# Performance work log

Hardware: AMD Instinct MI355X
Metric: run time of the kernel (lower is better)

The kernel has to match this reference:

```python
import jax, jax.numpy as jnp
from jax import lax
import numpy as np

SEQ, FEAT, VOCAB = 59, 64, 578
B, U = 4096, 1024


def setup_inputs() -> dict:
    key = jax.random.key(0)
    ks = jax.random.split(key, 6)
    x = jax.random.normal(ks[0], (B, SEQ, FEAT), dtype=jnp.float32)
    # Keras LSTMCell params: kernel [feat, 4U], recurrent_kernel [U, 4U], bias [4U]
    kernel = jax.random.normal(ks[1], (FEAT, 4 * U), dtype=jnp.float32) * 0.05
    rec_kernel = jax.random.normal(ks[2], (U, 4 * U), dtype=jnp.float32) * 0.05
    bias = jnp.zeros((4 * U,), dtype=jnp.float32)
    w2 = jax.random.normal(ks[3], (U, VOCAB), dtype=jnp.float32) * 0.05
    b2 = jnp.zeros((VOCAB,), dtype=jnp.float32)
    return {"x": x, "kernel": kernel, "rec_kernel": rec_kernel, "bias": bias, "w2": w2, "b2": b2}


def reference(x, kernel, rec_kernel, bias, w2, b2):
    batch = x.shape[0]
    units = rec_kernel.shape[0]
    xs = jnp.transpose(x, (1, 0, 2))  # [SEQ, B, FEAT]
    h0 = jnp.zeros((batch, units), dtype=x.dtype)
    c0 = jnp.zeros((batch, units), dtype=x.dtype)

    def step(carry, xt):
        h, c = carry
        z = xt @ kernel + h @ rec_kernel + bias  # [B, 4U]
        i, f, g, o = jnp.split(z, 4, axis=-1)    # Keras gate order i,f,c,o
        i = jax.nn.sigmoid(i)
        f = jax.nn.sigmoid(f)
        g = jnp.tanh(g)
        o = jax.nn.sigmoid(o)
        c_new = f * c + i * g
        h_new = o * jnp.tanh(c_new)
        return (h_new, c_new), None

    (h_last, _), _ = lax.scan(step, (h0, c0), xs)
    probs = jax.nn.softmax(h_last @ w2 + b2, axis=-1)  # dense2 softmax on last hidden
    # original: stack single prediction -> [1,B,V], transpose [1,0,2] -> [B,1,V]
    return probs[:, None, :]
```

## Files before the change

kernel.cpp:

```cpp
#include <hip/hip_runtime.h>

#define SEQ    59
#define FEAT   64
#define VOCAB  578
#define BATCH  4096
#define UNITS  1024
#define KLSTM  1088
#define KPAD   1152
#define HSTRIDE 1088
#define NPAD   640

typedef __bf16 bf16x8 __attribute__((ext_vector_type(8)));
typedef __bf16 bf16x4 __attribute__((ext_vector_type(4)));
typedef float  floatx4 __attribute__((ext_vector_type(4)));

typedef const __attribute__((address_space(1))) char gas_char;
typedef __attribute__((address_space(3))) char las_char;

__device__ __forceinline__ float sigmoid_f(float x) { return 1.f / (1.f + __expf(-x)); }
__device__ __forceinline__ float tanh_f(float x) { float e = __expf(2.f * x); return 1.f - 2.f / (e + 1.f); }

#define GLDS(srcp, dstp) __builtin_amdgcn_global_load_lds((gas_char*)(srcp), (las_char*)(dstp), 16, 0, 0)
#define BAR()  __builtin_amdgcn_s_barrier()
#define LGKM0() asm volatile("s_waitcnt lgkmcnt(0)" ::: "memory")
#define VM6()  asm volatile("s_waitcnt vmcnt(6)" ::: "memory")
#define MFMA   __builtin_amdgcn_mfma_f32_16x16x32_bf16


__global__ void convert_x_kernel(const float* __restrict__ x, __bf16* __restrict__ xbf) {
    int i = blockIdx.x * 256 + threadIdx.x;
    const int total = BATCH * SEQ * FEAT / 4;
    if (i >= total) return;
    float4 v = ((const float4*)x)[i];
    bf16x4 o;
    o.x = (__bf16)v.x; o.y = (__bf16)v.y; o.z = (__bf16)v.z; o.w = (__bf16)v.w;
    ((bf16x4*)xbf)[i] = o;
}

__global__ void convert_weights_kernel(const float* __restrict__ kern,
                                       const float* __restrict__ reck,
                                       __bf16* __restrict__ Wtp) {
    int idx = blockIdx.x * 256 + threadIdx.x;
    if (idx >= 4096 * KPAD) return;
    int np = idx / KPAD;
    int k  = idx - np * KPAD;
    int bc = np >> 8;
    int w  = (np >> 6) & 3;
    int g  = (np >> 4) & 3;
    int j  = np & 15;
    int n  = g * 1024 + bc * 64 + w * 16 + j;
    float v = 0.f;
    if (k < FEAT)       v = kern[(size_t)k * 4096 + n];
    else if (k < KLSTM) v = reck[(size_t)(k - FEAT) * 4096 + n];
    Wtp[idx] = (__bf16)v;
}

__global__ void convert_w2_kernel(const float* __restrict__ w2, __bf16* __restrict__ Wt2p) {
    int idx = blockIdx.x * 256 + threadIdx.x;
    if (idx >= NPAD * 1024) return;
    int n = idx >> 10;
    int k = idx & 1023;
    float v = (n < VOCAB) ? w2[(size_t)k * VOCAB + n] : 0.f;
    Wt2p[idx] = (__bf16)v;
}

__global__ void __launch_bounds__(512, 2) lstm_step_kernel(
    const __bf16* __restrict__ xbf,
    const __bf16* __restrict__ Wtp,
    const float*  __restrict__ bias,
    const __bf16* __restrict__ hin,
    __bf16*       __restrict__ hout,
    float*        __restrict__ cstate,
    int t)
{
    __shared__ __bf16 Ash[2][2][256 * 32];
    __shared__ __bf16 Bsh[2][2][128 * 64];

    const int tid  = threadIdx.x;
    const int wid  = tid >> 6;
    const int lane = tid & 63;
    const int ln   = lane & 15;
    const int lk   = lane >> 4;
    const int wm   = wid >> 2;
    const int wn   = wid & 3;
    const int rb   = blockIdx.x;
    const int bc   = blockIdx.y;

    floatx4 acc[8][4];
#pragma unroll
    for (int m = 0; m < 8; ++m)
#pragma unroll
        for (int g = 0; g < 4; ++g)
            acc[m][g] = (floatx4){0.f, 0.f, 0.f, 0.f};

    const int af0 = tid, af1 = 512 + tid;
    const int ar0 = af0 >> 2, ar1 = af1 >> 2;
    const int ac0 = (af0 & 3) ^ ((ar0 >> 1) & 3);
    const int ac1 = (af1 & 3) ^ ((ar1 >> 1) & 3);
    const int br0 = af0 >> 3, br1 = af1 >> 3;
    const int bc0 = (af0 & 7) ^ (br0 & 7);
    const int bc1 = (af1 & 7) ^ (br1 & 7);

    const __bf16* hA0 = hin + (size_t)(rb * 256 + ar0) * HSTRIDE + ac0 * 8;
    const __bf16* hA1 = hin + (size_t)(rb * 256 + ar1) * HSTRIDE + ac1 * 8;
    const __bf16* xA0 = xbf + (size_t)(rb * 256 + ar0) * (SEQ * FEAT) + t * FEAT + ac0 * 8;
    const __bf16* xA1 = xbf + (size_t)(rb * 256 + ar1) * (SEQ * FEAT) + t * FEAT + ac1 * 8;
    const __bf16* wB0 = Wtp + (size_t)(bc * 256 + br0) * KPAD + bc0 * 8;
    const __bf16* wB1 = Wtp + (size_t)(bc * 256 + br1) * KPAD + bc1 * 8;

    const int adst0 = (wid << 9);
    const int adst1 = 4096 + (wid << 9);

#define STA(BUF, KH, COLB) do { \
    GLDS(hA0 + (COLB) + (KH) * 32, &Ash[BUF][KH][adst0]); \
    GLDS(hA1 + (COLB) + (KH) * 32, &Ash[BUF][KH][adst1]); } while (0)
#define STB(BUF, NH, COLB) do { \
    GLDS(wB0 + (size_t)(NH) * 128 * KPAD + (COLB), &Bsh[BUF][NH][adst0]); \
    GLDS(wB1 + (size_t)(NH) * 128 * KPAD + (COLB), &Bsh[BUF][NH][adst1]); } while (0)

    int offA[8];
#pragma unroll
    for (int m = 0; m < 8; ++m) {
        int row = wm * 128 + m * 16 + ln;
        offA[m] = row * 32 + ((lk ^ ((row >> 1) & 3)) << 3);
    }
    int offB[4][2];
#pragma unroll
    for (int g = 0; g < 4; ++g) {
        int nr = (wn & 1) * 64 + g * 16 + ln;
#pragma unroll
        for (int kk = 0; kk < 2; ++kk)
            offB[g][kk] = nr * 64 + ((((kk << 2) + lk) ^ (nr & 7)) << 3);
    }
    const int nhsel = wn >> 1;
    const __bf16* B0  = Bsh[0][nhsel];
    const __bf16* B1  = Bsh[1][nhsel];
    const __bf16* A00 = Ash[0][0];
    const __bf16* A01 = Ash[0][1];
    const __bf16* A10 = Ash[1][0];
    const __bf16* A11 = Ash[1][1];

    STB(0, 1, 0);
    GLDS(xA0, &Ash[0][0][adst0]); GLDS(xA1, &Ash[0][0][adst1]);
    STB(0, 0, 0);
    GLDS(xA0 + 32, &Ash[0][1][adst0]); GLDS(xA1 + 32, &Ash[0][1][adst1]);
    STB(1, 1, 64);
    STA(1, 0, 0);
    STB(1, 0, 64);
    VM6();
    BAR();

#define PHASE_MFMA(MB, KKB) \
    __builtin_amdgcn_s_setprio(1); \
    _Pragma("unroll") \
    for (int m = 0; m < 4; ++m) \
    _Pragma("unroll") \
        for (int g = 0; g < 4; ++g) \
            acc[(MB) + m][g] = MFMA(aa[m], bb[KKB][g], acc[(MB) + m][g], 0, 0, 0); \
    __builtin_amdgcn_s_setprio(0)

#pragma unroll 1
    for (int it = 0; it < 9; ++it) {
        const int t2 = (2 * it + 2 <= 17) ? (2 * it + 2) : 17;
        const int t3 = (2 * it + 3 <= 17) ? (2 * it + 3) : 17;
        const int cA1 = it * 128;
        const int cB2 = t2 * 64, cA2 = (t2 - 1) * 64;
        const int cB3 = t3 * 64, cA3 = (t3 - 1) * 64;
        bf16x8 bb[2][4], aa[4];

#pragma unroll
        for (int g = 0; g < 4; ++g) {
            bb[0][g] = *(const bf16x8*)(B0 + offB[g][0]);
            bb[1][g] = *(const bf16x8*)(B0 + offB[g][1]);
        }
#pragma unroll
        for (int m = 0; m < 4; ++m) aa[m] = *(const bf16x8*)(A00 + offA[m]);
        STA(1, 1, cA1);
        BAR(); LGKM0();
        PHASE_MFMA(0, 0);
        BAR();
#pragma unroll
        for (int m = 0; m < 4; ++m) aa[m] = *(const bf16x8*)(A00 + offA[4 + m]);
        STB(0, 1, cB2);
        BAR(); LGKM0();
        PHASE_MFMA(4, 0);
        BAR();
#pragma unroll
        for (int m = 0; m < 4; ++m) aa[m] = *(const bf16x8*)(A01 + offA[m]);
        STA(0, 0, cA2);
        BAR(); LGKM0();
        PHASE_MFMA(0, 1);
        BAR();
#pragma unroll
        for (int m = 0; m < 4; ++m) aa[m] = *(const bf16x8*)(A01 + offA[4 + m]);
        STB(0, 0, cB2);
        BAR(); LGKM0();
        PHASE_MFMA(4, 1);
        VM6();
        BAR();

#pragma unroll
        for (int g = 0; g < 4; ++g) {
            bb[0][g] = *(const bf16x8*)(B1 + offB[g][0]);
            bb[1][g] = *(const bf16x8*)(B1 + offB[g][1]);
        }
#pragma unroll
        for (int m = 0; m < 4; ++m) aa[m] = *(const bf16x8*)(A10 + offA[m]);
        STA(0, 1, cA2);
        BAR(); LGKM0();
        PHASE_MFMA(0, 0);
        BAR();
#pragma unroll
        for (int m = 0; m < 4; ++m) aa[m] = *(const bf16x8*)(A10 + offA[4 + m]);
        STB(1, 1, cB3);
        BAR(); LGKM0();
        PHASE_MFMA(4, 0);
        BAR();
#pragma unroll
        for (int m = 0; m < 4; ++m) aa[m] = *(const bf16x8*)(A11 + offA[m]);
        STA(1, 0, cA3);
        BAR(); LGKM0();
        PHASE_MFMA(0, 1);
        BAR();
#pragma unroll
        for (int m = 0; m < 4; ++m) aa[m] = *(const bf16x8*)(A11 + offA[4 + m]);
        STB(1, 0, cB3);
        BAR(); LGKM0();
        PHASE_MFMA(4, 1);
        VM6();
        BAR();
    }

    asm volatile("s_waitcnt vmcnt(0)" ::: "memory");

    const int u = bc * 64 + wn * 16 + ln;
    const float bi  = bias[u];
    const float bfv = bias[UNITS + u];
    const float bg  = bias[2 * UNITS + u];
    const float bo  = bias[3 * UNITS + u];
#pragma unroll
    for (int m = 0; m < 8; ++m) {
        const int row0 = rb * 256 + wm * 128 + m * 16 + lk * 4;
#pragma unroll
        for (int r = 0; r < 4; ++r) {
            const size_t ic = (size_t)(row0 + r) * UNITS + u;
            float ig = sigmoid_f(acc[m][0][r] + bi);
            float fg = sigmoid_f(acc[m][1][r] + bfv);
            float gg = tanh_f(acc[m][2][r] + bg);
            float og = sigmoid_f(acc[m][3][r] + bo);
            float cn = fg * cstate[ic] + ig * gg;
            cstate[ic] = cn;
            hout[(size_t)(row0 + r) * HSTRIDE + u] = (__bf16)(og * tanh_f(cn));
        }
    }
#undef STA
#undef STB
}

__global__ void __launch_bounds__(256) dense_kernel(
    const __bf16* __restrict__ hin,
    const __bf16* __restrict__ Wt2p,
    float*        __restrict__ logits)
{
    __shared__ __bf16 As[128 * 64];
    __shared__ __bf16 Bs[128 * 64];

    const int tid  = threadIdx.x;
    const int wid  = tid >> 6;
    const int lane = tid & 63;
    const int ln   = lane & 15;
    const int lk   = lane >> 4;
    const int wm   = wid >> 1;
    const int wn   = wid & 1;
    const int rb   = blockIdx.x;
    const int nb   = blockIdx.y;

    floatx4 acc[4][4];
#pragma unroll
    for (int m = 0; m < 4; ++m)
#pragma unroll
        for (int g = 0; g < 4; ++g)
            acc[m][g] = (floatx4){0.f, 0.f, 0.f, 0.f};

    int s_row[4], s_kgd[4];
#pragma unroll
    for (int q = 0; q < 4; ++q) {
        int flat = q * 256 + tid;
        int row  = flat >> 3;
        s_row[q] = row;
        s_kgd[q] = (flat & 7) ^ (row & 7);
    }

    for (int kt = 0; kt < 16; ++kt) {
        __syncthreads();
#pragma unroll
        for (int q = 0; q < 4; ++q) {
            const int row = s_row[q], kgd = s_kgd[q];
            const __bf16* gp = hin + (size_t)(rb * 128 + row) * HSTRIDE + kt * 64 + kgd * 8;
            GLDS(gp, As + (size_t)(q * 256 + (wid << 6)) * 8);
        }
#pragma unroll
        for (int q = 0; q < 4; ++q) {
            const int n = s_row[q], kgd = s_kgd[q];
            const __bf16* gp = Wt2p + ((size_t)(nb * 128 + n) << 10) + kt * 64 + kgd * 8;
            GLDS(gp, Bs + (size_t)(q * 256 + (wid << 6)) * 8);
        }
        __syncthreads();
#pragma unroll
        for (int kk = 0; kk < 2; ++kk) {
            const int kg = kk * 4 + lk;
            bf16x8 a[4], b[4];
#pragma unroll
            for (int m = 0; m < 4; ++m) {
                int row  = wm * 64 + m * 16 + ln;
                int ccol = (kg ^ (row & 7)) * 8;
                a[m] = *(const bf16x8*)(As + row * 64 + ccol);
            }
#pragma unroll
            for (int g = 0; g < 4; ++g) {
                int n    = g * 32 + wn * 16 + ln;
                int ccol = (kg ^ (n & 7)) * 8;
                b[g] = *(const bf16x8*)(Bs + n * 64 + ccol);
            }
#pragma unroll
            for (int m = 0; m < 4; ++m)
#pragma unroll
                for (int g = 0; g < 4; ++g)
                    acc[m][g] = MFMA(a[m], b[g], acc[m][g], 0, 0, 0);
        }
    }

#pragma unroll
    for (int m = 0; m < 4; ++m) {
        const int row0 = rb * 128 + wm * 64 + m * 16 + lk * 4;
#pragma unroll
        for (int g = 0; g < 4; ++g) {
            const int n = nb * 128 + g * 32 + wn * 16 + ln;
#pragma unroll
            for (int r = 0; r < 4; ++r)
                logits[(size_t)(row0 + r) * NPAD + n] = acc[m][g][r];
        }
    }
}

__global__ void __launch_bounds__(256) softmax_kernel(
    const float* __restrict__ logits,
    const float* __restrict__ b2,
    float* __restrict__ out)
{
    const int row = blockIdx.x;
    const int tid = threadIdx.x;
    __shared__ float red[8];

    float z[3];
    float lmax = -1e30f;
#pragma unroll
    for (int j = 0; j < 3; ++j) {
        int col = tid + j * 256;
        if (col < VOCAB) {
            z[j] = logits[(size_t)row * NPAD + col] + b2[col];
            lmax = fmaxf(lmax, z[j]);
        } else z[j] = -1e30f;
    }
    for (int off = 32; off > 0; off >>= 1) lmax = fmaxf(lmax, __shfl_xor(lmax, off));
    if ((tid & 63) == 0) red[tid >> 6] = lmax;
    __syncthreads();
    lmax = fmaxf(fmaxf(red[0], red[1]), fmaxf(red[2], red[3]));
    __syncthreads();

    float lsum = 0.f;
#pragma unroll
    for (int j = 0; j < 3; ++j) {
        int col = tid + j * 256;
        if (col < VOCAB) { z[j] = __expf(z[j] - lmax); lsum += z[j]; }
    }
    for (int off = 32; off > 0; off >>= 1) lsum += __shfl_xor(lsum, off);
    if ((tid & 63) == 0) red[tid >> 6] = lsum;
    __syncthreads();
    lsum = red[0] + red[1] + red[2] + red[3];
    float inv = 1.f / lsum;
#pragma unroll
    for (int j = 0; j < 3; ++j) {
        int col = tid + j * 256;
        if (col < VOCAB) out[(size_t)row * VOCAB + col] = z[j] * inv;
    }
}

extern "C" void kernel_launch(void* const* d_in, const int* in_sizes, int n_in,
                              void* d_out, int out_size, void* d_ws, size_t ws_size,
                              hipStream_t stream)
{
    const float* x    = (const float*)d_in[0];
    const float* kern = (const float*)d_in[1];
    const float* reck = (const float*)d_in[2];
    const float* bias = (const float*)d_in[3];
    const float* w2   = (const float*)d_in[4];
    const float* b2   = (const float*)d_in[5];
    float* out = (float*)d_out;

    char* ws = (char*)d_ws;
    size_t off = 0;
    auto alloc = [&](size_t bytes) {
        char* p = ws + off;
        off += (bytes + 255) & ~(size_t)255;
        return p;
    };
    __bf16* Wtp    = (__bf16*)alloc((size_t)4096 * KPAD * 2);
    __bf16* Wt2p   = (__bf16*)alloc((size_t)NPAD * 1024 * 2);
    __bf16* xbf    = (__bf16*)alloc((size_t)BATCH * SEQ * FEAT * 2);
    __bf16* h0     = (__bf16*)alloc((size_t)BATCH * HSTRIDE * 2);
    __bf16* h1     = (__bf16*)alloc((size_t)BATCH * HSTRIDE * 2);
    float*  cst    = (float*)alloc((size_t)BATCH * UNITS * 4);
    float*  logits = (float*)alloc((size_t)BATCH * NPAD * 4);
    if (off > ws_size) return;

    (void)hipMemsetAsync(h0, 0, (size_t)BATCH * HSTRIDE * 2, stream);
    (void)hipMemsetAsync(h1, 0, (size_t)BATCH * HSTRIDE * 2, stream);
    (void)hipMemsetAsync(cst, 0, (size_t)BATCH * UNITS * 4, stream);

    convert_x_kernel<<<(BATCH * SEQ * FEAT / 4 + 255) / 256, 256, 0, stream>>>(x, xbf);
    convert_weights_kernel<<<(4096 * KPAD + 255) / 256, 256, 0, stream>>>(kern, reck, Wtp);
    convert_w2_kernel<<<(NPAD * 1024 + 255) / 256, 256, 0, stream>>>(w2, Wt2p);

    __bf16* hin = h0; __bf16* hout = h1;
    for (int t = 0; t < SEQ; ++t) {
        lstm_step_kernel<<<dim3(16, 16), 512, 0, stream>>>(xbf, Wtp, bias, hin, hout, cst, t);
        __bf16* tmp = hin; hin = hout; hout = tmp;
    }

    dense_kernel<<<dim3(32, 5), 256, 0, stream>>>(hin, Wt2p, logits);
    softmax_kernel<<<BATCH, 256, 0, stream>>>(logits, b2, out);
}
```

Measured before the change: 2.832 ms.

## Fuse all LSTM timesteps into one persistent kernel with grid barrier

Replaces the 59 per-timestep kernel launches with a single persistent kernel that loops over timesteps and synchronises all 256 blocks through an atomic-counter grid barrier. The cell state now stays in registers instead of being read from and written to global memory each step, and the weight and x tiles for the next step are prefetched before the barrier. The padded strides are dropped for h and weights. The cost is that the spin barrier requires all 256 blocks to be co-resident, and it serialises on one global atomic.

```diff
diff --git a/kernel.cpp b/kernel.cpp
--- a/kernel.cpp
+++ b/kernel.cpp
@@ -6,9 +6,8 @@
 #define BATCH  4096
 #define UNITS  1024
 #define KLSTM  1088
-#define KPAD   1152
-#define HSTRIDE 1088
 #define NPAD   640
+#define NBLK   256
 
 typedef __bf16 bf16x8 __attribute__((ext_vector_type(8)));
 typedef __bf16 bf16x4 __attribute__((ext_vector_type(4)));
@@ -21,10 +20,10 @@
 __device__ __forceinline__ float tanh_f(float x) { float e = __expf(2.f * x); return 1.f - 2.f / (e + 1.f); }
 
 #define GLDS(srcp, dstp) __builtin_amdgcn_global_load_lds((gas_char*)(srcp), (las_char*)(dstp), 16, 0, 0)
-#define BAR()  __builtin_amdgcn_s_barrier()
+#define BAR()   __builtin_amdgcn_s_barrier()
 #define LGKM0() asm volatile("s_waitcnt lgkmcnt(0)" ::: "memory")
-#define VM6()  asm volatile("s_waitcnt vmcnt(6)" ::: "memory")
-#define MFMA   __builtin_amdgcn_mfma_f32_16x16x32_bf16
+#define VMW(n)  asm volatile("s_waitcnt vmcnt(" #n ")" ::: "memory")
+#define MFMA    __builtin_amdgcn_mfma_f32_16x16x32_bf16
 
 
 __global__ void convert_x_kernel(const float* __restrict__ x, __bf16* __restrict__ xbf) {
@@ -41,17 +40,16 @@
                                        const float* __restrict__ reck,
                                        __bf16* __restrict__ Wtp) {
     int idx = blockIdx.x * 256 + threadIdx.x;
-    if (idx >= 4096 * KPAD) return;
-    int np = idx / KPAD;
-    int k  = idx - np * KPAD;
+    if (idx >= 4096 * KLSTM) return;
+    int np = idx / KLSTM;
+    int k  = idx - np * KLSTM;
     int bc = np >> 8;
     int w  = (np >> 6) & 3;
     int g  = (np >> 4) & 3;
     int j  = np & 15;
     int n  = g * 1024 + bc * 64 + w * 16 + j;
-    float v = 0.f;
-    if (k < FEAT)       v = kern[(size_t)k * 4096 + n];
-    else if (k < KLSTM) v = reck[(size_t)(k - FEAT) * 4096 + n];
+    float v = (k < FEAT) ? kern[(size_t)k * 4096 + n]
+                         : reck[(size_t)(k - FEAT) * 4096 + n];
     Wtp[idx] = (__bf16)v;
 }
 
@@ -64,14 +62,13 @@
     Wt2p[idx] = (__bf16)v;
 }
 
-__global__ void __launch_bounds__(512, 2) lstm_step_kernel(
+__global__ void __launch_bounds__(512, 2) lstm_seq_kernel(
     const __bf16* __restrict__ xbf,
     const __bf16* __restrict__ Wtp,
     const float*  __restrict__ bias,
-    const __bf16* __restrict__ hin,
-    __bf16*       __restrict__ hout,
-    float*        __restrict__ cstate,
-    int t)
+    __bf16*       __restrict__ hb0,
+    __bf16*       __restrict__ hb1,
+    unsigned*                  barcnt)
 {
     __shared__ __bf16 Ash[2][2][256 * 32];
     __shared__ __bf16 Bsh[2][2][128 * 64];
@@ -83,40 +80,26 @@
     const int lk   = lane >> 4;
     const int wm   = wid >> 2;
     const int wn   = wid & 3;
-    const int rb   = blockIdx.x;
-    const int bc   = blockIdx.y;
-
-    floatx4 acc[8][4];
-#pragma unroll
-    for (int m = 0; m < 8; ++m)
-#pragma unroll
-        for (int g = 0; g < 4; ++g)
-            acc[m][g] = (floatx4){0.f, 0.f, 0.f, 0.f};
+    const int bc   = blockIdx.x;
+    const int rb   = blockIdx.y;
 
     const int af0 = tid, af1 = 512 + tid;
     const int ar0 = af0 >> 2, ar1 = af1 >> 2;
     const int ac0 = (af0 & 3) ^ ((ar0 >> 1) & 3);
     const int ac1 = (af1 & 3) ^ ((ar1 >> 1) & 3);
     const int br0 = af0 >> 3, br1 = af1 >> 3;
-    const int bc0 = (af0 & 7) ^ (br0 & 7);
-    const int bc1 = (af1 & 7) ^ (br1 & 7);
-
-    const __bf16* hA0 = hin + (size_t)(rb * 256 + ar0) * HSTRIDE + ac0 * 8;
-    const __bf16* hA1 = hin + (size_t)(rb * 256 + ar1) * HSTRIDE + ac1 * 8;
-    const __bf16* xA0 = xbf + (size_t)(rb * 256 + ar0) * (SEQ * FEAT) + t * FEAT + ac0 * 8;
-    const __bf16* xA1 = xbf + (size_t)(rb * 256 + ar1) * (SEQ * FEAT) + t * FEAT + ac1 * 8;
-    const __bf16* wB0 = Wtp + (size_t)(bc * 256 + br0) * KPAD + bc0 * 8;
-    const __bf16* wB1 = Wtp + (size_t)(bc * 256 + br1) * KPAD + bc1 * 8;
-
-    const int adst0 = (wid << 9);
+    const int bq0 = (af0 & 7) ^ (br0 & 7);
+    const int bq1 = (af1 & 7) ^ (br1 & 7);
+
+    const __bf16* wB0 = Wtp + (size_t)(bc * 256 + br0) * KLSTM + bq0 * 8;
+    const __bf16* wB1 = Wtp + (size_t)(bc * 256 + br1) * KLSTM + bq1 * 8;
+    const __bf16* xr0 = xbf + (size_t)(rb * 256 + ar0) * (SEQ * FEAT) + ac0 * 8;
+    const __bf16* xr1 = xbf + (size_t)(rb * 256 + ar1) * (SEQ * FEAT) + ac1 * 8;
+    const size_t  ho0 = (size_t)(rb * 256 + ar0) * UNITS + ac0 * 8;
+    const size_t  ho1 = (size_t)(rb * 256 + ar1) * UNITS + ac1 * 8;
+
+    const int adst0 = wid << 9;
     const int adst1 = 4096 + (wid << 9);
-
-#define STA(BUF, KH, COLB) do { \
-    GLDS(hA0 + (COLB) + (KH) * 32, &Ash[BUF][KH][adst0]); \
-    GLDS(hA1 + (COLB) + (KH) * 32, &Ash[BUF][KH][adst1]); } while (0)
-#define STB(BUF, NH, COLB) do { \
-    GLDS(wB0 + (size_t)(NH) * 128 * KPAD + (COLB), &Bsh[BUF][NH][adst0]); \
-    GLDS(wB1 + (size_t)(NH) * 128 * KPAD + (COLB), &Bsh[BUF][NH][adst1]); } while (0)
 
     int offA[8];
 #pragma unroll
@@ -140,16 +123,26 @@
     const __bf16* A10 = Ash[1][0];
     const __bf16* A11 = Ash[1][1];
 
-    STB(0, 1, 0);
-    GLDS(xA0, &Ash[0][0][adst0]); GLDS(xA1, &Ash[0][0][adst1]);
-    STB(0, 0, 0);
-    GLDS(xA0 + 32, &Ash[0][1][adst0]); GLDS(xA1 + 32, &Ash[0][1][adst1]);
-    STB(1, 1, 64);
-    STA(1, 0, 0);
-    STB(1, 0, 64);
-    VM6();
-    BAR();
-
+    const int u = bc * 64 + wn * 16 + ln;
+    const float bi  = bias[u];
+    const float bfv = bias[UNITS + u];
+    const float bg  = bias[2 * UNITS + u];
+    const float bo  = bias[3 * UNITS + u];
+
+    float cc[8][4];
+#pragma unroll
+    for (int m = 0; m < 8; ++m)
+#pragma unroll
+        for (int r = 0; r < 4; ++r) cc[m][r] = 0.f;
+
+    floatx4 acc[8][4];
+
+#define STAH(BUF, KH, T) do { const int _c = ((T) - 1) * 64 + (KH) * 32; \
+    GLDS(hA0 + _c, &Ash[BUF][KH][adst0]); \
+    GLDS(hA1 + _c, &Ash[BUF][KH][adst1]); } while (0)
+#define STBT(BUF, NH, T) do { const size_t _c = (size_t)(NH) * 128 * KLSTM + (T) * 64; \
+    GLDS(wB0 + _c, &Bsh[BUF][NH][adst0]); \
+    GLDS(wB1 + _c, &Bsh[BUF][NH][adst1]); } while (0)
 #define PHASE_MFMA(MB, KKB) \
     __builtin_amdgcn_s_setprio(1); \
     _Pragma("unroll") \
@@ -160,101 +153,137 @@
     __builtin_amdgcn_s_setprio(0)
 
 #pragma unroll 1
-    for (int it = 0; it < 9; ++it) {
-        const int t2 = (2 * it + 2 <= 17) ? (2 * it + 2) : 17;
-        const int t3 = (2 * it + 3 <= 17) ? (2 * it + 3) : 17;
-        const int cA1 = it * 128;
-        const int cB2 = t2 * 64, cA2 = (t2 - 1) * 64;
-        const int cB3 = t3 * 64, cA3 = (t3 - 1) * 64;
-        bf16x8 bb[2][4], aa[4];
-
-#pragma unroll
-        for (int g = 0; g < 4; ++g) {
-            bb[0][g] = *(const bf16x8*)(B0 + offB[g][0]);
-            bb[1][g] = *(const bf16x8*)(B0 + offB[g][1]);
-        }
-#pragma unroll
-        for (int m = 0; m < 4; ++m) aa[m] = *(const bf16x8*)(A00 + offA[m]);
-        STA(1, 1, cA1);
-        BAR(); LGKM0();
-        PHASE_MFMA(0, 0);
+    for (int t = 0; t < SEQ; ++t) {
+        const __bf16* hin  = (t & 1) ? hb1 : hb0;
+        __bf16*       hout = (t & 1) ? hb0 : hb1;
+        const __bf16* hA0  = hin + ho0;
+        const __bf16* hA1  = hin + ho1;
+        const __bf16* xA0  = xr0 + t * FEAT;
+        const __bf16* xA1  = xr1 + t * FEAT;
+
+#pragma unroll
+        for (int m = 0; m < 8; ++m)
+#pragma unroll
+            for (int g = 0; g < 4; ++g)
+                acc[m][g] = (floatx4){0.f, 0.f, 0.f, 0.f};
+
+        STBT(0, 1, 0);
+        GLDS(xA0, &Ash[0][0][adst0]); GLDS(xA1, &Ash[0][0][adst1]);
+        STBT(0, 0, 0);
+        GLDS(xA0 + 32, &Ash[0][1][adst0]); GLDS(xA1 + 32, &Ash[0][1][adst1]);
+        STBT(1, 1, 1);
+        STBT(1, 0, 1);
+
+        __threadfence();
+        __syncthreads();
+        if (tid == 0) {
+            __hip_atomic_fetch_add(barcnt, 1u, __ATOMIC_ACQ_REL, __HIP_MEMORY_SCOPE_AGENT);
+            const unsigned tgt = (unsigned)(t + 1) * NBLK;
+            while (__hip_atomic_load(barcnt, __ATOMIC_RELAXED, __HIP_MEMORY_SCOPE_AGENT) < tgt)
+                __builtin_amdgcn_s_sleep(2);
+            (void)__hip_atomic_load(barcnt, __ATOMIC_ACQUIRE, __HIP_MEMORY_SCOPE_AGENT);
+        }
+        __syncthreads();
+
+        STAH(1, 0, 1);
+        STAH(1, 1, 1);
+        VMW(8);
         BAR();
-#pragma unroll
-        for (int m = 0; m < 4; ++m) aa[m] = *(const bf16x8*)(A00 + offA[4 + m]);
-        STB(0, 1, cB2);
-        BAR(); LGKM0();
-        PHASE_MFMA(4, 0);
+        {
+            bf16x8 bb[2][4], aa[4];
+#pragma unroll
+            for (int g = 0; g < 4; ++g) {
+                bb[0][g] = *(const bf16x8*)(B0 + offB[g][0]);
+                bb[1][g] = *(const bf16x8*)(B0 + offB[g][1]);
+            }
+#pragma unroll
+            for (int m = 0; m < 4; ++m) aa[m] = *(const bf16x8*)(A00 + offA[m]);
+            LGKM0(); PHASE_MFMA(0, 0);
+#pragma unroll
+            for (int m = 0; m < 4; ++m) aa[m] = *(const bf16x8*)(A00 + offA[4 + m]);
+            LGKM0(); PHASE_MFMA(4, 0);
+#pragma unroll
+            for (int m = 0; m < 4; ++m) aa[m] = *(const bf16x8*)(A01 + offA[m]);
+            LGKM0(); PHASE_MFMA(0, 1);
+#pragma unroll
+            for (int m = 0; m < 4; ++m) aa[m] = *(const bf16x8*)(A01 + offA[4 + m]);
+            LGKM0(); PHASE_MFMA(4, 1);
+        }
         BAR();
-#pragma unroll
-        for (int m = 0; m < 4; ++m) aa[m] = *(const bf16x8*)(A01 + offA[m]);
-        STA(0, 0, cA2);
-        BAR(); LGKM0();
-        PHASE_MFMA(0, 1);
+        STBT(0, 1, 2);
+        STAH(0, 0, 2);
+        STBT(0, 0, 2);
+        VMW(6);
         BAR();
-#pragma unroll
-        for (int m = 0; m < 4; ++m) aa[m] = *(const bf16x8*)(A01 + offA[4 + m]);
-        STB(0, 0, cB2);
-        BAR(); LGKM0();
-        PHASE_MFMA(4, 1);
-        VM6();
-        BAR();
-
-#pragma unroll
-        for (int g = 0; g < 4; ++g) {
-            bb[0][g] = *(const bf16x8*)(B1 + offB[g][0]);
-            bb[1][g] = *(const bf16x8*)(B1 + offB[g][1]);
-        }
-#pragma unroll
-        for (int m = 0; m < 4; ++m) aa[m] = *(const bf16x8*)(A10 + offA[m]);
-        STA(0, 1, cA2);
-        BAR(); LGKM0();
-        PHASE_MFMA(0, 0);
-        BAR();
-#pragma unroll
-        for (int m = 0; m < 4; ++m) aa[m] = *(const bf16x8*)(A10 + offA[4 + m]);
-        STB(1, 1, cB3);
-        BAR(); LGKM0();
-        PHASE_MFMA(4, 0);
-        BAR();
-#pragma unroll
-        for (int m = 0; m < 4; ++m) aa[m] = *(const bf16x8*)(A11 + offA[m]);
-        STA(1, 0, cA3);
-        BAR(); LGKM0();
-        PHASE_MFMA(0, 1);
-        BAR();
-#pragma unroll
-        for (int m = 0; m < 4; ++m) aa[m] = *(const bf16x8*)(A11 + offA[4 + m]);
-        STB(1, 0, cB3);
-        BAR(); LGKM0();
-        PHASE_MFMA(4, 1);
-        VM6();
-        BAR();
-    }
-
-    asm volatile("s_waitcnt vmcnt(0)" ::: "memory");
-
-    const int u = bc * 64 + wn * 16 + ln;
-    const float bi  = bias[u];
-    const float bfv = bias[UNITS + u];
-    const float bg  = bias[2 * UNITS + u];
-    const float bo  = bias[3 * UNITS + u];
-#pragma unroll
-    for (int m = 0; m < 8; ++m) {
-        const int row0 = rb * 256 + wm * 128 + m * 16 + lk * 4;
-#pragma unroll
-        for (int r = 0; r < 4; ++r) {
-            const size_t ic = (size_t)(row0 + r) * UNITS + u;
-            float ig = sigmoid_f(acc[m][0][r] + bi);
-            float fg = sigmoid_f(acc[m][1][r] + bfv);
-            float gg = tanh_f(acc[m][2][r] + bg);
-            float og = sigmoid_f(acc[m][3][r] + bo);
-            float cn = fg * cstate[ic] + ig * gg;
-            cstate[ic] = cn;
-            hout[(size_t)(row0 + r) * HSTRIDE + u] = (__bf16)(og * tanh_f(cn));
-        }
-    }
-#undef STA
-#undef STB
+
+#pragma unroll 1
+        for (int it = 0; it < 8; ++it) {
+            const int T2 = 2 * it + 2;
+            const int T3 = (2 * it + 3 < 17) ? (2 * it + 3) : 16;
+            const int T4 = (2 * it + 4 < 17) ? (2 * it + 4) : 16;
+            bf16x8 bb[2][4], aa[4];
+#pragma unroll
+            for (int g = 0; g < 4; ++g) {
+                bb[0][g] = *(const bf16x8*)(B1 + offB[g][0]);
+                bb[1][g] = *(const bf16x8*)(B1 + offB[g][1]);
+            }
+#pragma unroll
+            for (int m = 0; m < 4; ++m) aa[m] = *(const bf16x8*)(A10 + offA[m]);
+            STAH(0, 1, T2);
+            BAR(); LGKM0(); PHASE_MFMA(0, 0); BAR();
+#pragma unroll
+            for (int m = 0; m < 4; ++m) aa[m] = *(const bf16x8*)(A10 + offA[4 + m]);
+            STBT(1, 1, T3);
+            BAR(); LGKM0(); PHASE_MFMA(4, 0); BAR();
+#pragma unroll
+            for (int m = 0; m < 4; ++m) aa[m] = *(const bf16x8*)(A11 + offA[m]);
+            STAH(1, 0, T3);
+            BAR(); LGKM0(); PHASE_MFMA(0, 1); BAR();
+#pragma unroll
+            for (int m = 0; m < 4; ++m) aa[m] = *(const bf16x8*)(A11 + offA[4 + m]);
+            STBT(1, 0, T3);
+            BAR(); LGKM0(); PHASE_MFMA(4, 1); VMW(6); BAR();
+#pragma unroll
+            for (int g = 0; g < 4; ++g) {
+                bb[0][g] = *(const bf16x8*)(B0 + offB[g][0]);
+                bb[1][g] = *(const bf16x8*)(B0 + offB[g][1]);
+            }
+#pragma unroll
+            for (int m = 0; m < 4; ++m) aa[m] = *(const bf16x8*)(A00 + offA[m]);
+            STAH(1, 1, T3);
+            BAR(); LGKM0(); PHASE_MFMA(0, 0); BAR();
+#pragma unroll
+            for (int m = 0; m < 4; ++m) aa[m] = *(const bf16x8*)(A00 + offA[4 + m]);
+            STBT(0, 1, T4);
+            BAR(); LGKM0(); PHASE_MFMA(4, 0); BAR();
+#pragma unroll
+            for (int m = 0; m < 4; ++m) aa[m] = *(const bf16x8*)(A01 + offA[m]);
+            STAH(0, 0, T4);
+            BAR(); LGKM0(); PHASE_MFMA(0, 1); BAR();
+#pragma unroll
+            for (int m = 0; m < 4; ++m) aa[m] = *(const bf16x8*)(A01 + offA[4 + m]);
+            STBT(0, 0, T4);
+            BAR(); LGKM0(); PHASE_MFMA(4, 1); VMW(6); BAR();
+        }
+        VMW(0);
+
+#pragma unroll
+        for (int m = 0; m < 8; ++m) {
+            const int row0 = rb * 256 + wm * 128 + m * 16 + lk * 4;
+#pragma unroll
+            for (int r = 0; r < 4; ++r) {
+                float ig = sigmoid_f(acc[m][0][r] + bi);
+                float fg = sigmoid_f(acc[m][1][r] + bfv);
+                float gg = tanh_f(acc[m][2][r] + bg);
+                float og = sigmoid_f(acc[m][3][r] + bo);
+                float cn = fg * cc[m][r] + ig * gg;
+                cc[m][r] = cn;
+                hout[(size_t)(row0 + r) * UNITS + u] = (__bf16)(og * tanh_f(cn));
+            }
+        }
+    }
+#undef STAH
+#undef STBT
 }
 
 __global__ void __launch_bounds__(256) dense_kernel(
@@ -296,7 +325,7 @@
 #pragma unroll
         for (int q = 0; q < 4; ++q) {
             const int row = s_row[q], kgd = s_kgd[q];
-            const __bf16* gp = hin + (size_t)(rb * 128 + row) * HSTRIDE + kt * 64 + kgd * 8;
+            const __bf16* gp = hin + ((size_t)(rb * 128 + row) << 10) + kt * 64 + kgd * 8;
             GLDS(gp, As + (size_t)(q * 256 + (wid << 6)) * 8);
         }
 #pragma unroll
@@ -405,29 +434,24 @@
         off += (bytes + 255) & ~(size_t)255;
         return p;
     };
-    __bf16* Wtp    = (__bf16*)alloc((size_t)4096 * KPAD * 2);
-    __bf16* Wt2p   = (__bf16*)alloc((size_t)NPAD * 1024 * 2);
-    __bf16* xbf    = (__bf16*)alloc((size_t)BATCH * SEQ * FEAT * 2);
-    __bf16* h0     = (__bf16*)alloc((size_t)BATCH * HSTRIDE * 2);
-    __bf16* h1     = (__bf16*)alloc((size_t)BATCH * HSTRIDE * 2);
-    float*  cst    = (float*)alloc((size_t)BATCH * UNITS * 4);
-    float*  logits = (float*)alloc((size_t)BATCH * NPAD * 4);
+    __bf16*   Wtp    = (__bf16*)alloc((size_t)4096 * KLSTM * 2);
+    __bf16*   Wt2p   = (__bf16*)alloc((size_t)NPAD * 1024 * 2);
+    __bf16*   xbf    = (__bf16*)alloc((size_t)BATCH * SEQ * FEAT * 2);
+    __bf16*   h0     = (__bf16*)alloc((size_t)BATCH * UNITS * 2);
+    __bf16*   h1     = (__bf16*)alloc((size_t)BATCH * UNITS * 2);
+    float*    logits = (float*)alloc((size_t)BATCH * NPAD * 4);
+    unsigned* barcnt = (unsigned*)alloc(256);
     if (off > ws_size) return;
 
-    (void)hipMemsetAsync(h0, 0, (size_t)BATCH * HSTRIDE * 2, stream);
-    (void)hipMemsetAsync(h1, 0, (size_t)BATCH * HSTRIDE * 2, stream);
-    (void)hipMemsetAsync(cst, 0, (size_t)BATCH * UNITS * 4, stream);
+    (void)hipMemsetAsync(h0, 0, (size_t)BATCH * UNITS * 2, stream);
+    (void)hipMemsetAsync(barcnt, 0, 256, stream);
 
     convert_x_kernel<<<(BATCH * SEQ * FEAT / 4 + 255) / 256, 256, 0, stream>>>(x, xbf);
-    convert_weights_kernel<<<(4096 * KPAD + 255) / 256, 256, 0, stream>>>(kern, reck, Wtp);
+    convert_weights_kernel<<<(4096 * KLSTM + 255) / 256, 256, 0, stream>>>(kern, reck, Wtp);
     convert_w2_kernel<<<(NPAD * 1024 + 255) / 256, 256, 0, stream>>>(w2, Wt2p);
 
-    __bf16* hin = h0; __bf16* hout = h1;
-    for (int t = 0; t < SEQ; ++t) {
-        lstm_step_kernel<<<dim3(16, 16), 512, 0, stream>>>(xbf, Wtp, bias, hin, hout, cst, t);
-        __bf16* tmp = hin; hin = hout; hout = tmp;
-    }
-
-    dense_kernel<<<dim3(32, 5), 256, 0, stream>>>(hin, Wt2p, logits);
+    lstm_seq_kernel<<<dim3(16, 16), 512, 0, stream>>>(xbf, Wtp, bias, h0, h1, barcnt);
+
+    dense_kernel<<<dim3(32, 5), 256, 0, stream>>>(h1, Wt2p, logits);
     softmax_kernel<<<BATCH, 256, 0, stream>>>(logits, b2, out);
 }
```

Measured after the change: 7.955 ms. 2.81x slower.
